# Optimization experiments

Measured on AMD Instinct MI355X. Metric: run time of the kernel, lower is better.

## Reference

```python
import jax, jax.numpy as jnp
import numpy as np

N, E = 100000, 1600000
IN_C, OUT_C, H, EDGE_DIM = 128, 64, 2, 4
NEG_SLOPE = 0.2
LN_EPS = 1e-5


def setup_inputs() -> dict:
    key = jax.random.key(0)
    ks = jax.random.split(key, 12)
    s = 1.0 / np.sqrt(IN_C)
    inp = {
        "x": jax.random.normal(ks[0], (N, IN_C), jnp.float32),
        "edge_index": jax.random.randint(ks[1], (2, E), 0, N, jnp.int64),
        "edge_attr": jax.random.normal(ks[2], (E, EDGE_DIM), jnp.float32),
        "W": jax.random.normal(ks[3], (IN_C, H * OUT_C), jnp.float32) * s,
        "att_src": jax.random.normal(ks[4], (H, OUT_C), jnp.float32) * s,
        "att_dst": jax.random.normal(ks[5], (H, OUT_C), jnp.float32) * s,
        "W_edge": jax.random.normal(ks[6], (EDGE_DIM, H * OUT_C), jnp.float32) * 0.5,
        "att_edge": jax.random.normal(ks[7], (H, OUT_C), jnp.float32) * s,
        "bias": jnp.zeros((OUT_C,), jnp.float32),
        "gamma": jnp.ones((OUT_C,), jnp.float32),
        "beta": jnp.zeros((OUT_C,), jnp.float32),
    }
    return inp


def reference(x, edge_index, edge_attr, W, att_src, att_dst, W_edge, att_edge, bias, gamma, beta):
    n = x.shape[0]
    src, dst = edge_index[0], edge_index[1]
    # shared src/dst linear (PyG GATConv with single input tensor)
    h = (x @ W).reshape(n, H, OUT_C)                       # [N,H,C]
    a_src = jnp.einsum("nhc,hc->nh", h, att_src)          # [N,H]
    a_dst = jnp.einsum("nhc,hc->nh", h, att_dst)          # [N,H]
    e = (edge_attr @ W_edge).reshape(-1, H, OUT_C)         # [E,H,C]
    a_edge = jnp.einsum("ehc,hc->eh", e, att_edge)        # [E,H]
    alpha = jax.nn.leaky_relu(a_src[src] + a_dst[dst] + a_edge, NEG_SLOPE)  # [E,H]
    # segment softmax over edges grouped by destination node
    amax = jax.ops.segment_max(alpha, dst, num_segments=n)
    ex = jnp.exp(alpha - amax[dst])
    denom = jax.ops.segment_sum(ex, dst, num_segments=n)
    w = ex / (denom[dst] + 1e-16)                          # [E,H]
    msg = h[src] * w[:, :, None]                           # [E,H,C]
    out = jax.ops.segment_sum(msg, dst, num_segments=n)    # [N,H,C]
    out = out.mean(axis=1) + bias                          # concat=False -> head mean
    # LayerNorm + ReLU
    mu = out.mean(-1, keepdims=True)
    var = ((out - mu) ** 2).mean(-1, keepdims=True)
    out = (out - mu) * jax.lax.rsqrt(var + LN_EPS) * gamma + beta
    return jax.nn.relu(out)
```

## Files before the change

### kernel.cpp

```cpp
#include <hip/hip_runtime.h>
#include <hip/hip_fp16.h>
#include <math.h>

#define IN_C 128
#define HC   128
#define OUT_C 64
#define NEG_SLOPE 0.2f
#define LN_EPS 1e-5f
#define CHUNK 8192
#define NBMAX 1024

typedef __attribute__((ext_vector_type(8))) short bf16x8;
typedef __attribute__((ext_vector_type(4))) float f32x4;

__device__ inline unsigned bf16pack(float a, float b) {
    unsigned ua = __float_as_uint(a), ub = __float_as_uint(b);
    ua = (ua + 0x7fffu + ((ua >> 16) & 1u)) >> 16;
    ub = (ub + 0x7fffu + ((ub >> 16) & 1u)) >> 16;
    return ua | (ub << 16);
}

__global__ __launch_bounds__(256) void k_pre(const float* __restrict__ W,
                                             const float* __restrict__ W_edge,
                                             const float* __restrict__ att_edge,
                                             const int* __restrict__ ei_dst,
                                             unsigned short* __restrict__ WbfT,
                                             float* __restrict__ V,
                                             int* __restrict__ off,
                                             int E, int NB, int PB) {
    __shared__ int hist[NBMAX];
    int b = blockIdx.x, t = threadIdx.x;
    if (b < 8) {
        #pragma unroll
        for (int i = 0; i < 8; ++i) {
            int idx = b * 2048 + i * 256 + t;
            int k = idx >> 7, col = idx & 127;
            unsigned u = __float_as_uint(W[idx]);
            WbfT[col * 128 + k] =
                (unsigned short)((u + 0x7fffu + ((u >> 16) & 1u)) >> 16);
        }
        return;
    }
    if (b == 8) {
        if (t < 8) {
            int d = t >> 1, h = t & 1;
            float s = 0.f;
            for (int c = 0; c < 64; ++c)
                s += W_edge[d * HC + h * 64 + c] * att_edge[h * 64 + c];
            V[d * 2 + h] = s;
        }
        return;
    }
    int pb = b - 9;
    for (int i = t; i < NB; i += 256) hist[i] = 0;
    __syncthreads();
    int base = pb * CHUNK;
    int lim = E - base; if (lim > CHUNK) lim = CHUNK;
    for (int i4 = t; i4 * 4 < lim; i4 += 256) {
        int idx = base + i4 * 4;
        if (idx + 3 < base + lim) {
            int4 v = *(const int4*)&ei_dst[idx];
            atomicAdd(&hist[v.x >> 7], 1);
            atomicAdd(&hist[v.y >> 7], 1);
            atomicAdd(&hist[v.z >> 7], 1);
            atomicAdd(&hist[v.w >> 7], 1);
        } else {
            for (int k = idx; k < base + lim; ++k)
                atomicAdd(&hist[ei_dst[k] >> 7], 1);
        }
    }
    __syncthreads();
    for (int i = t; i < NB; i += 256)
        off[(size_t)i * PB + pb] = hist[i];
}

__global__ __launch_bounds__(256) void k_mid(const float* __restrict__ x,
                                             const unsigned short* __restrict__ WbfT,
                                             const float* __restrict__ attS,
                                             const float* __restrict__ attD,
                                             unsigned* __restrict__ hb,
                                             float* __restrict__ a_src,
                                             float* __restrict__ a_dst, int M,
                                             int* __restrict__ off,
                                             int* __restrict__ bsum,
                                             int nS, int GB) {
    __shared__ unsigned xb[64 * 64];
    const int t = threadIdx.x;
    const int bid = blockIdx.x;

    if (bid >= GB) {
        int* sm = (int*)xb;
        int blk = bid - GB;
        int base = blk * 1024 + t * 4;
        int v0 = 0, v1 = 0, v2 = 0, v3 = 0;
        if (base + 0 < nS) v0 = off[base + 0];
        if (base + 1 < nS) v1 = off[base + 1];
        if (base + 2 < nS) v2 = off[base + 2];
        if (base + 3 < nS) v3 = off[base + 3];
        int s = v0 + v1 + v2 + v3;
        sm[t] = s;
        __syncthreads();
        for (int o = 1; o < 256; o <<= 1) {
            int u = (t >= o) ? sm[t - o] : 0;
            __syncthreads();
            sm[t] += u;
            __syncthreads();
        }
        int excl = sm[t] - s;
        if (base + 0 < nS) off[base + 0] = excl;
        if (base + 1 < nS) off[base + 1] = excl + v0;
        if (base + 2 < nS) off[base + 2] = excl + v0 + v1;
        if (base + 3 < nS) off[base + 3] = excl + v0 + v1 + v2;
        if (t == 255) bsum[blk] = sm[255];
        return;
    }

    const int brow = bid * 64;
    const float4* x4 = (const float4*)x;
    #pragma unroll
    for (int i = 0; i < 8; ++i) {
        int idx = i * 256 + t;
        int row = idx >> 5, c4 = idx & 31;
        float4 v = make_float4(0.f, 0.f, 0.f, 0.f);
        if (brow + row < M) v = x4[(size_t)(brow + row) * 32 + c4];
        unsigned lo = bf16pack(v.x, v.y), hi = bf16pack(v.z, v.w);
        int byte = row * 256 + ((c4 * 8) ^ ((row & 7) << 4));
        *(uint2*)((char*)xb + byte) = make_uint2(lo, hi);
    }
    __syncthreads();

    const int w = t >> 6, lane = t & 63;
    const int col = lane & 15, qr = lane >> 4;
    f32x4 acc[8];
    #pragma unroll
    for (int ct = 0; ct < 8; ++ct) acc[ct] = (f32x4){0.f, 0.f, 0.f, 0.f};

    const int arow = w * 16 + col;
    #pragma unroll
    for (int ks = 0; ks < 4; ++ks) {
        int abyte = arow * 256 + ((ks * 64 + qr * 16) ^ ((arow & 7) << 4));
        bf16x8 af = *(const bf16x8*)((const char*)xb + abyte);
        #pragma unroll
        for (int ct = 0; ct < 8; ++ct) {
            bf16x8 bfr = *(const bf16x8*)&WbfT[(size_t)(ct * 16 + col) * 128 + ks * 32 + qr * 8];
            acc[ct] = __builtin_amdgcn_mfma_f32_16x16x32_bf16(af, bfr, acc[ct], 0, 0, 0);
        }
    }

    float pS0[4], pS1[4], pD0[4], pD1[4];
    #pragma unroll
    for (int r = 0; r < 4; ++r) { pS0[r] = pS1[r] = pD0[r] = pD1[r] = 0.f; }
    #pragma unroll
    for (int ct = 0; ct < 8; ++ct) {
        float s = attS[ct * 16 + col], d = attD[ct * 16 + col];
        #pragma unroll
        for (int r = 0; r < 4; ++r) {
            float a = acc[ct][r];
            if (ct < 4) { pS0[r] += a * s; pD0[r] += a * d; }
            else        { pS1[r] += a * s; pD1[r] += a * d; }
        }
    }
    #pragma unroll
    for (int m = 1; m < 16; m <<= 1) {
        #pragma unroll
        for (int r = 0; r < 4; ++r) {
            pS0[r] += __shfl_xor(pS0[r], m);
            pS1[r] += __shfl_xor(pS1[r], m);
            pD0[r] += __shfl_xor(pD0[r], m);
            pD1[r] += __shfl_xor(pD1[r], m);
        }
    }
    #pragma unroll
    for (int r = 0; r < 4; ++r) {
        int grow = brow + w * 16 + qr * 4 + r;
        if (grow < M) {
            if (col == 0) {
                a_src[2 * grow + 0] = pS0[r];
                a_src[2 * grow + 1] = pS1[r];
                a_dst[2 * grow + 0] = pD0[r];
                a_dst[2 * grow + 1] = pD1[r];
            }
            #pragma unroll
            for (int ct = 0; ct < 4; ++ct)
                hb[(size_t)grow * 64 + ct * 16 + col] =
                    bf16pack(acc[ct][r], acc[ct + 4][r]);
        }
    }
}

__global__ __launch_bounds__(256) void k_part(const int* __restrict__ ei,
                                              const float* __restrict__ ea,
                                              const float* __restrict__ V,
                                              const float* __restrict__ a_src,
                                              const float* __restrict__ a_dst,
                                              const int* __restrict__ off,
                                              const int* __restrict__ bsum,
                                              int* __restrict__ bsum2,
                                              uint2* __restrict__ pA,
                                              int E, int NB, int PB, int nb2) {
    __shared__ int cur[NBMAX];
    __shared__ int bs[256];
    int pb = blockIdx.x, t = threadIdx.x;

    int r0 = (t < nb2) ? bsum[t] : 0;
    bs[t] = r0;
    __syncthreads();
    for (int o = 1; o < 256; o <<= 1) {
        int u = (t >= o) ? bs[t - o] : 0;
        __syncthreads();
        bs[t] += u;
        __syncthreads();
    }
    bs[t] -= r0;
    __syncthreads();
    if (pb == 0 && t < nb2) bsum2[t] = bs[t];

    for (int i = t; i < NB; i += 256) {
        size_t oi = (size_t)i * PB + pb;
        cur[i] = off[oi] + bs[(int)(oi >> 10)];
    }
    __syncthreads();
    float v0 = V[0], v1 = V[1], v2 = V[2], v3 = V[3];
    float v4 = V[4], v5 = V[5], v6 = V[6], v7 = V[7];
    int base = pb * CHUNK;
    int lim = E - base; if (lim > CHUNK) lim = CHUNK;
    #pragma unroll 2
    for (int i = t; i < lim; i += 256) {
        int e = base + i;
        int s = ei[e], d = ei[E + e];
        float4 a = ((const float4*)ea)[e];
        float ae0 = a.x * v0 + a.y * v2 + a.z * v4 + a.w * v6;
        float ae1 = a.x * v1 + a.y * v3 + a.z * v5 + a.w * v7;
        float2 as = ((const float2*)a_src)[s];
        float2 ad = ((const float2*)a_dst)[d];
        float al0 = as.x + ad.x + ae0; al0 = al0 > 0.f ? al0 : NEG_SLOPE * al0;
        float al1 = as.y + ad.y + ae1; al1 = al1 > 0.f ? al1 : NEG_SLOPE * al1;
        __half2 hx = __floats2half2_rn(__expf(al0), __expf(al1));
        int slot = atomicAdd(&cur[d >> 7], 1);
        pA[slot] = make_uint2((unsigned)s | ((unsigned)(d & 127) << 17),
                              *reinterpret_cast<unsigned*>(&hx));
    }
}

__global__ __launch_bounds__(256) void k_csr(const uint2* __restrict__ pA,
                                             const int* __restrict__ off,
                                             const int* __restrict__ bsum2,
                                             int* __restrict__ rowptr,
                                             uint2* __restrict__ payload,
                                             int M, int E, int NB, int PB) {
    __shared__ int cnt[128];
    __shared__ int sc[128];
    __shared__ int cur[128];
    int b = blockIdx.x, t = threadIdx.x;
    int n0 = b << 7;
    int nloc = M - n0; if (nloc > 128) nloc = 128;

    size_t o0 = (size_t)b * PB;
    int s0 = off[o0] + bsum2[(int)(o0 >> 10)];
    int s1 = E;
    if (b + 1 < NB) {
        size_t o1 = (size_t)(b + 1) * PB;
        s1 = off[o1] + bsum2[(int)(o1 >> 10)];
    }
    if (t < 128) cnt[t] = 0;
    __syncthreads();

    for (int i = s0 + t; i < s1; i += 256)
        atomicAdd(&cnt[(pA[i].x >> 17) & 127], 1);
    __syncthreads();
    if (t < 128) sc[t] = cnt[t];
    __syncthreads();
    for (int o = 1; o < 128; o <<= 1) {
        int u = 0;
        if (t < 128 && t >= o) u = sc[t - o];
        __syncthreads();
        if (t < 128) sc[t] += u;
        __syncthreads();
    }
    if (t < 128) {
        int base = s0 + sc[t] - cnt[t];
        cur[t] = base;
        if (t < nloc) rowptr[n0 + t] = base;
    }
    if (b == NB - 1 && t == 0) rowptr[M] = E;
    __syncthreads();
    for (int i = s0 + t; i < s1; i += 256) {
        uint2 p = pA[i];
        int dl = (p.x >> 17) & 127;
        int pos = atomicAdd(&cur[dl], 1);
        payload[pos] = make_uint2(p.x & 0x1FFFF, p.y);
    }
}

__global__ __launch_bounds__(256) void k_gather(const uint2* __restrict__ payload,
                                                const int* __restrict__ rowptr,
                                                const unsigned* __restrict__ hb,
                                                const float* __restrict__ bias,
                                                const float* __restrict__ gamma,
                                                const float* __restrict__ beta,
                                                float* __restrict__ out, int M) {
    __shared__ uint2 stg[4][64];
    int w = threadIdx.x >> 6, lane = threadIdx.x & 63;
    int n = blockIdx.x * 4 + w;
    if (n >= M) return;
    int beg = rowptr[n], end = rowptr[n + 1];
    float acc0 = 0.f, acc1 = 0.f, pe0 = 0.f, pe1 = 0.f;

    for (int base = beg; base < end; base += 64) {
        int cnt = end - base; if (cnt > 64) cnt = 64;
        uint2 p = make_uint2(0u, 0u);
        if (lane < cnt) p = payload[base + lane];
        stg[w][lane] = p;
        {
            __half2 he = *reinterpret_cast<__half2*>(&p.y);
            pe0 += __low2float(he);
            pe1 += __high2float(he);
        }
        int j = 0;
        for (; j + 8 <= cnt; j += 8) {
            uint2 q0 = stg[w][j + 0], q1 = stg[w][j + 1];
            uint2 q2 = stg[w][j + 2], q3 = stg[w][j + 3];
            uint2 q4 = stg[w][j + 4], q5 = stg[w][j + 5];
            uint2 q6 = stg[w][j + 6], q7 = stg[w][j + 7];
            int s0 = __builtin_amdgcn_readfirstlane((int)q0.x);
            int s1 = __builtin_amdgcn_readfirstlane((int)q1.x);
            int s2 = __builtin_amdgcn_readfirstlane((int)q2.x);
            int s3 = __builtin_amdgcn_readfirstlane((int)q3.x);
            int s4 = __builtin_amdgcn_readfirstlane((int)q4.x);
            int s5 = __builtin_amdgcn_readfirstlane((int)q5.x);
            int s6 = __builtin_amdgcn_readfirstlane((int)q6.x);
            int s7 = __builtin_amdgcn_readfirstlane((int)q7.x);
            unsigned h0 = (hb + (size_t)s0 * 64)[lane];
            unsigned h1 = (hb + (size_t)s1 * 64)[lane];
            unsigned h2 = (hb + (size_t)s2 * 64)[lane];
            unsigned h3 = (hb + (size_t)s3 * 64)[lane];
            unsigned h4 = (hb + (size_t)s4 * 64)[lane];
            unsigned h5 = (hb + (size_t)s5 * 64)[lane];
            unsigned h6 = (hb + (size_t)s6 * 64)[lane];
            unsigned h7 = (hb + (size_t)s7 * 64)[lane];
            __half2 e0 = *reinterpret_cast<__half2*>(&q0.y);
            __half2 e1 = *reinterpret_cast<__half2*>(&q1.y);
            __half2 e2 = *reinterpret_cast<__half2*>(&q2.y);
            __half2 e3 = *reinterpret_cast<__half2*>(&q3.y);
            __half2 e4 = *reinterpret_cast<__half2*>(&q4.y);
            __half2 e5 = *reinterpret_cast<__half2*>(&q5.y);
            __half2 e6 = *reinterpret_cast<__half2*>(&q6.y);
            __half2 e7 = *reinterpret_cast<__half2*>(&q7.y);
            acc0 += __low2float(e0)  * __uint_as_float(h0 << 16);
            acc1 += __high2float(e0) * __uint_as_float(h0 & 0xffff0000u);
            acc0 += __low2float(e1)  * __uint_as_float(h1 << 16);
            acc1 += __high2float(e1) * __uint_as_float(h1 & 0xffff0000u);
            acc0 += __low2float(e2)  * __uint_as_float(h2 << 16);
            acc1 += __high2float(e2) * __uint_as_float(h2 & 0xffff0000u);
            acc0 += __low2float(e3)  * __uint_as_float(h3 << 16);
            acc1 += __high2float(e3) * __uint_as_float(h3 & 0xffff0000u);
            acc0 += __low2float(e4)  * __uint_as_float(h4 << 16);
            acc1 += __high2float(e4) * __uint_as_float(h4 & 0xffff0000u);
            acc0 += __low2float(e5)  * __uint_as_float(h5 << 16);
            acc1 += __high2float(e5) * __uint_as_float(h5 & 0xffff0000u);
            acc0 += __low2float(e6)  * __uint_as_float(h6 << 16);
            acc1 += __high2float(e6) * __uint_as_float(h6 & 0xffff0000u);
            acc0 += __low2float(e7)  * __uint_as_float(h7 << 16);
            acc1 += __high2float(e7) * __uint_as_float(h7 & 0xffff0000u);
        }
        for (; j + 4 <= cnt; j += 4) {
            uint2 q0 = stg[w][j + 0], q1 = stg[w][j + 1];
            uint2 q2 = stg[w][j + 2], q3 = stg[w][j + 3];
            int s0 = __builtin_amdgcn_readfirstlane((int)q0.x);
            int s1 = __builtin_amdgcn_readfirstlane((int)q1.x);
            int s2 = __builtin_amdgcn_readfirstlane((int)q2.x);
            int s3 = __builtin_amdgcn_readfirstlane((int)q3.x);
            unsigned h0 = (hb + (size_t)s0 * 64)[lane];
            unsigned h1 = (hb + (size_t)s1 * 64)[lane];
            unsigned h2 = (hb + (size_t)s2 * 64)[lane];
            unsigned h3 = (hb + (size_t)s3 * 64)[lane];
            __half2 e0 = *reinterpret_cast<__half2*>(&q0.y);
            __half2 e1 = *reinterpret_cast<__half2*>(&q1.y);
            __half2 e2 = *reinterpret_cast<__half2*>(&q2.y);
            __half2 e3 = *reinterpret_cast<__half2*>(&q3.y);
            acc0 += __low2float(e0)  * __uint_as_float(h0 << 16);
            acc1 += __high2float(e0) * __uint_as_float(h0 & 0xffff0000u);
            acc0 += __low2float(e1)  * __uint_as_float(h1 << 16);
            acc1 += __high2float(e1) * __uint_as_float(h1 & 0xffff0000u);
            acc0 += __low2float(e2)  * __uint_as_float(h2 << 16);
            acc1 += __high2float(e2) * __uint_as_float(h2 & 0xffff0000u);
            acc0 += __low2float(e3)  * __uint_as_float(h3 << 16);
            acc1 += __high2float(e3) * __uint_as_float(h3 & 0xffff0000u);
        }
        for (; j < cnt; ++j) {
            uint2 q0 = stg[w][j];
            int s0 = __builtin_amdgcn_readfirstlane((int)q0.x);
            unsigned h0 = (hb + (size_t)s0 * 64)[lane];
            __half2 e0 = *reinterpret_cast<__half2*>(&q0.y);
            acc0 += __low2float(e0)  * __uint_as_float(h0 << 16);
            acc1 += __high2float(e0) * __uint_as_float(h0 & 0xffff0000u);
        }
    }

    float d0 = pe0, d1 = pe1;
    #pragma unroll
    for (int m = 32; m; m >>= 1) {
        d0 += __shfl_xor(d0, m);
        d1 += __shfl_xor(d1, m);
    }

    float o = 0.5f * (acc0 / (d0 + 1e-16f) + acc1 / (d1 + 1e-16f)) + bias[lane];
    float mu = o;
    #pragma unroll
    for (int m = 32; m; m >>= 1) mu += __shfl_xor(mu, m);
    mu *= (1.f / 64.f);
    float c = o - mu;
    float v = c * c;
    #pragma unroll
    for (int m = 32; m; m >>= 1) v += __shfl_xor(v, m);
    v *= (1.f / 64.f);
    float y = c * rsqrtf(v + LN_EPS) * gamma[lane] + beta[lane];
    out[(size_t)n * OUT_C + lane] = fmaxf(y, 0.f);
}

extern "C" void kernel_launch(void* const* d_in, const int* in_sizes, int n_in,
                              void* d_out, int out_size, void* d_ws, size_t ws_size,
                              hipStream_t stream) {
    const float* x     = (const float*)d_in[0];
    const int*   ei    = (const int*)d_in[1];
    const float* ea    = (const float*)d_in[2];
    const float* W     = (const float*)d_in[3];
    const float* attS  = (const float*)d_in[4];
    const float* attD  = (const float*)d_in[5];
    const float* We    = (const float*)d_in[6];
    const float* attE  = (const float*)d_in[7];
    const float* bias  = (const float*)d_in[8];
    const float* gamma = (const float*)d_in[9];
    const float* beta  = (const float*)d_in[10];

    const int M  = in_sizes[0] / IN_C;
    const int E  = in_sizes[1] / 2;
    const int NB = (M + 127) >> 7;
    const int PB = (E + CHUNK - 1) / CHUNK;
    const int nS = NB * PB;
    const int nb2 = (nS + 1023) / 1024;
    const int GB = (M + 63) / 64;

    char* ws = (char*)d_ws;
    size_t woff = 0;
    auto alloc = [&](size_t bytes) -> void* {
        void* p = ws + woff;
        woff += (bytes + 255) & ~(size_t)255;
        return p;
    };
    unsigned*       hb     = (unsigned*)      alloc((size_t)M * 64 * 4);
    float*          a_src  = (float*)         alloc((size_t)M * 2 * 4);
    float*          a_dst  = (float*)         alloc((size_t)M * 2 * 4);
    int*            off    = (int*)           alloc((size_t)nS * 4);
    int*            bsum   = (int*)           alloc((size_t)nb2 * 4);
    int*            bsum2  = (int*)           alloc((size_t)nb2 * 4);
    int*            rowptr = (int*)           alloc((size_t)(M + 1) * 4);
    uint2*          pA     = (uint2*)         alloc((size_t)E * 8);
    uint2*          payload= (uint2*)         alloc((size_t)E * 8);
    unsigned short* WbfT   = (unsigned short*)alloc(128 * 128 * 2);
    float*          V      = (float*)         alloc(32);

    k_pre<<<9 + PB, 256, 0, stream>>>(W, We, attE, ei + E, WbfT, V, off, E, NB, PB);
    k_mid<<<GB + nb2, 256, 0, stream>>>(x, WbfT, attS, attD, hb, a_src, a_dst, M,
                                        off, bsum, nS, GB);
    k_part<<<PB, 256, 0, stream>>>(ei, ea, V, a_src, a_dst, off, bsum, bsum2,
                                   pA, E, NB, PB, nb2);
    k_csr<<<NB, 256, 0, stream>>>(pA, off, bsum2, rowptr, payload, M, E, NB, PB);
    k_gather<<<(M + 3) / 4, 256, 0, stream>>>(payload, rowptr, hb, bias, gamma, beta,
                                              (float*)d_out, M);
}
```

Measured before the change: 161.8 us.

## Shrink partition chunks and batch edge loads for more memory parallelism

```diff
diff --git a/kernel.cpp b/kernel.cpp
--- a/kernel.cpp
+++ b/kernel.cpp
@@ -7,8 +7,9 @@
 #define OUT_C 64
 #define NEG_SLOPE 0.2f
 #define LN_EPS 1e-5f
-#define CHUNK 8192
+#define CHUNK 2048
 #define NBMAX 1024
+#define NB2MAX 1024
 
 typedef __attribute__((ext_vector_type(8))) short bf16x8;
 typedef __attribute__((ext_vector_type(4))) float f32x4;
@@ -56,18 +57,20 @@
     __syncthreads();
     int base = pb * CHUNK;
     int lim = E - base; if (lim > CHUNK) lim = CHUNK;
-    for (int i4 = t; i4 * 4 < lim; i4 += 256) {
-        int idx = base + i4 * 4;
-        if (idx + 3 < base + lim) {
-            int4 v = *(const int4*)&ei_dst[idx];
-            atomicAdd(&hist[v.x >> 7], 1);
-            atomicAdd(&hist[v.y >> 7], 1);
-            atomicAdd(&hist[v.z >> 7], 1);
-            atomicAdd(&hist[v.w >> 7], 1);
-        } else {
-            for (int k = idx; k < base + lim; ++k)
-                atomicAdd(&hist[ei_dst[k] >> 7], 1);
-        }
+    if (lim == CHUNK) {
+        int4 v0 = *(const int4*)&ei_dst[base + t * 4];
+        int4 v1 = *(const int4*)&ei_dst[base + 1024 + t * 4];
+        atomicAdd(&hist[v0.x >> 7], 1);
+        atomicAdd(&hist[v0.y >> 7], 1);
+        atomicAdd(&hist[v0.z >> 7], 1);
+        atomicAdd(&hist[v0.w >> 7], 1);
+        atomicAdd(&hist[v1.x >> 7], 1);
+        atomicAdd(&hist[v1.y >> 7], 1);
+        atomicAdd(&hist[v1.z >> 7], 1);
+        atomicAdd(&hist[v1.w >> 7], 1);
+    } else {
+        for (int i = t; i < lim; i += 256)
+            atomicAdd(&hist[ei_dst[base + i] >> 7], 1);
     }
     __syncthreads();
     for (int i = t; i < NB; i += 256)
@@ -188,6 +191,29 @@
     }
 }
 
+__device__ inline void scan_bsum(const int* __restrict__ bsum, int nb2,
+                                 int* bs, int* sm, int t) {
+    int v0 = (4 * t + 0 < nb2) ? bsum[4 * t + 0] : 0;
+    int v1 = (4 * t + 1 < nb2) ? bsum[4 * t + 1] : 0;
+    int v2 = (4 * t + 2 < nb2) ? bsum[4 * t + 2] : 0;
+    int v3 = (4 * t + 3 < nb2) ? bsum[4 * t + 3] : 0;
+    int s = v0 + v1 + v2 + v3;
+    sm[t] = s;
+    __syncthreads();
+    for (int o = 1; o < 256; o <<= 1) {
+        int u = (t >= o) ? sm[t - o] : 0;
+        __syncthreads();
+        sm[t] += u;
+        __syncthreads();
+    }
+    int excl = sm[t] - s;
+    bs[4 * t + 0] = excl;
+    bs[4 * t + 1] = excl + v0;
+    bs[4 * t + 2] = excl + v0 + v1;
+    bs[4 * t + 3] = excl + v0 + v1 + v2;
+    __syncthreads();
+}
+
 __global__ __launch_bounds__(256) void k_part(const int* __restrict__ ei,
                                               const float* __restrict__ ea,
                                               const float* __restrict__ V,
@@ -199,21 +225,13 @@
                                               uint2* __restrict__ pA,
                                               int E, int NB, int PB, int nb2) {
     __shared__ int cur[NBMAX];
-    __shared__ int bs[256];
+    __shared__ int bs[NB2MAX];
+    __shared__ int sm[256];
     int pb = blockIdx.x, t = threadIdx.x;
 
-    int r0 = (t < nb2) ? bsum[t] : 0;
-    bs[t] = r0;
-    __syncthreads();
-    for (int o = 1; o < 256; o <<= 1) {
-        int u = (t >= o) ? bs[t - o] : 0;
-        __syncthreads();
-        bs[t] += u;
-        __syncthreads();
-    }
-    bs[t] -= r0;
-    __syncthreads();
-    if (pb == 0 && t < nb2) bsum2[t] = bs[t];
+    scan_bsum(bsum, nb2, bs, sm, t);
+    if (pb == 0)
+        for (int i = t; i < nb2; i += 256) bsum2[i] = bs[i];
 
     for (int i = t; i < NB; i += 256) {
         size_t oi = (size_t)i * PB + pb;
@@ -224,21 +242,53 @@
     float v4 = V[4], v5 = V[5], v6 = V[6], v7 = V[7];
     int base = pb * CHUNK;
     int lim = E - base; if (lim > CHUNK) lim = CHUNK;
-    #pragma unroll 2
-    for (int i = t; i < lim; i += 256) {
-        int e = base + i;
-        int s = ei[e], d = ei[E + e];
-        float4 a = ((const float4*)ea)[e];
-        float ae0 = a.x * v0 + a.y * v2 + a.z * v4 + a.w * v6;
-        float ae1 = a.x * v1 + a.y * v3 + a.z * v5 + a.w * v7;
-        float2 as = ((const float2*)a_src)[s];
-        float2 ad = ((const float2*)a_dst)[d];
-        float al0 = as.x + ad.x + ae0; al0 = al0 > 0.f ? al0 : NEG_SLOPE * al0;
-        float al1 = as.y + ad.y + ae1; al1 = al1 > 0.f ? al1 : NEG_SLOPE * al1;
-        __half2 hx = __floats2half2_rn(__expf(al0), __expf(al1));
-        int slot = atomicAdd(&cur[d >> 7], 1);
-        pA[slot] = make_uint2((unsigned)s | ((unsigned)(d & 127) << 17),
-                              *reinterpret_cast<unsigned*>(&hx));
+
+    if (lim == CHUNK) {
+        int e0 = base + t;
+        int sA[8], dA[8];
+        #pragma unroll
+        for (int k = 0; k < 8; ++k) {
+            sA[k] = ei[e0 + k * 256];
+            dA[k] = ei[E + e0 + k * 256];
+        }
+        float4 aA[8];
+        #pragma unroll
+        for (int k = 0; k < 8; ++k) aA[k] = ((const float4*)ea)[e0 + k * 256];
+        float2 asA[8], adA[8];
+        #pragma unroll
+        for (int k = 0; k < 8; ++k) {
+            asA[k] = ((const float2*)a_src)[sA[k]];
+            adA[k] = ((const float2*)a_dst)[dA[k]];
+        }
+        #pragma unroll
+        for (int k = 0; k < 8; ++k) {
+            float ae0 = aA[k].x * v0 + aA[k].y * v2 + aA[k].z * v4 + aA[k].w * v6;
+            float ae1 = aA[k].x * v1 + aA[k].y * v3 + aA[k].z * v5 + aA[k].w * v7;
+            float al0 = asA[k].x + adA[k].x + ae0;
+            al0 = al0 > 0.f ? al0 : NEG_SLOPE * al0;
+            float al1 = asA[k].y + adA[k].y + ae1;
+            al1 = al1 > 0.f ? al1 : NEG_SLOPE * al1;
+            __half2 hx = __floats2half2_rn(__expf(al0), __expf(al1));
+            int slot = atomicAdd(&cur[dA[k] >> 7], 1);
+            pA[slot] = make_uint2((unsigned)sA[k] | ((unsigned)(dA[k] & 127) << 17),
+                                  *reinterpret_cast<unsigned*>(&hx));
+        }
+    } else {
+        for (int i = t; i < lim; i += 256) {
+            int e = base + i;
+            int s = ei[e], d = ei[E + e];
+            float4 a = ((const float4*)ea)[e];
+            float ae0 = a.x * v0 + a.y * v2 + a.z * v4 + a.w * v6;
+            float ae1 = a.x * v1 + a.y * v3 + a.z * v5 + a.w * v7;
+            float2 as = ((const float2*)a_src)[s];
+            float2 ad = ((const float2*)a_dst)[d];
+            float al0 = as.x + ad.x + ae0; al0 = al0 > 0.f ? al0 : NEG_SLOPE * al0;
+            float al1 = as.y + ad.y + ae1; al1 = al1 > 0.f ? al1 : NEG_SLOPE * al1;
+            __half2 hx = __floats2half2_rn(__expf(al0), __expf(al1));
+            int slot = atomicAdd(&cur[d >> 7], 1);
+            pA[slot] = make_uint2((unsigned)s | ((unsigned)(d & 127) << 17),
+                                  *reinterpret_cast<unsigned*>(&hx));
+        }
     }
 }
 
```

New measurement: 170.8 us. 5.6% more time.
